# Kernel optimization log

Hardware: AMD Instinct MI355X
Metric: run time of the kernel (lower is better)

Reference implementation:

```python
import jax, jax.numpy as jnp
import numpy as np

N_NODES = 20000
IN_C = 512
OUT_C = 128
HEADS = 4
N_EDGES = 320000
NEG_SLOPE = 0.2


def setup_inputs() -> dict:
    key = jax.random.key(0)
    ks = jax.random.split(key, 10)
    x = jax.random.normal(ks[0], (N_NODES, IN_C), dtype=jnp.float32)
    edge_index = jax.random.randint(ks[1], (2, N_EDGES), 0, N_NODES, dtype=jnp.int64)
    s = 0.05
    return {
        "x": x,
        "edge_index": edge_index,
        "W1": jax.random.normal(ks[2], (IN_C, HEADS * OUT_C), dtype=jnp.float32) * s,
        "a_src1": jax.random.normal(ks[3], (HEADS, OUT_C), dtype=jnp.float32) * s,
        "a_dst1": jax.random.normal(ks[4], (HEADS, OUT_C), dtype=jnp.float32) * s,
        "b1": jnp.zeros((HEADS * OUT_C,), dtype=jnp.float32),
        "W2": jax.random.normal(ks[5], (HEADS * OUT_C, 1 * OUT_C), dtype=jnp.float32) * s,
        "a_src2": jax.random.normal(ks[6], (1, OUT_C), dtype=jnp.float32) * s,
        "a_dst2": jax.random.normal(ks[7], (1, OUT_C), dtype=jnp.float32) * s,
        "b2": jnp.zeros((OUT_C,), dtype=jnp.float32),
    }


def gat_conv(x, src, dst, W, a_src, a_dst, b, heads, out_c, concat):
    N = x.shape[0]
    h = (x @ W).reshape(N, heads, out_c)            # [N,H,C]
    al_src = jnp.sum(h * a_src, axis=-1)            # [N,H]
    al_dst = jnp.sum(h * a_dst, axis=-1)            # [N,H]
    e = jax.nn.leaky_relu(al_src[src] + al_dst[dst], NEG_SLOPE)  # [E,H]
    # segment softmax over edges grouped by destination node
    e_max = jax.ops.segment_max(e, dst, num_segments=N)         # [N,H]
    e = jnp.exp(e - e_max[dst])
    denom = jax.ops.segment_sum(e, dst, num_segments=N)         # [N,H]
    alpha = e / (denom[dst] + 1e-16)                             # [E,H]
    msg = h[src] * alpha[:, :, None]                             # [E,H,C]
    out = jax.ops.segment_sum(msg, dst, num_segments=N)          # [N,H,C]
    out = out.reshape(N, heads * out_c) if concat else jnp.mean(out, axis=1)
    return out + b


def reference(x, edge_index, W1, a_src1, a_dst1, b1, W2, a_src2, a_dst2, b2):
    N = x.shape[0]
    # PyG GATConv adds self-loops by default
    loops = jnp.arange(N, dtype=edge_index.dtype)
    src = jnp.concatenate([edge_index[0], loops])
    dst = jnp.concatenate([edge_index[1], loops])
    h = gat_conv(x, src, dst, W1, a_src1, a_dst1, b1, HEADS, OUT_C, concat=True)
    h = jax.nn.elu(h)
    return gat_conv(h, src, dst, W2, a_src2, a_dst2, b2, 1, OUT_C, concat=False)
```

## Files before the change

kernel.cpp:

```cpp
#include <hip/hip_runtime.h>
#include <hip/hip_bf16.h>

typedef __hip_bfloat16 bf16;
typedef __bf16 bf16x8 __attribute__((ext_vector_type(8)));
typedef float f32x4 __attribute__((ext_vector_type(4)));

#define NEG_SLOPE 0.2f
#define F32_THRESH 256


__device__ __forceinline__ bool is_f32(const int* fcnt) { return *fcnt > F32_THRESH; }

__device__ __forceinline__ float ld_f(const void* p, long long i, bool f32) {
    return f32 ? ((const float*)p)[i] : __bfloat162float(((const bf16*)p)[i]);
}

__device__ __forceinline__ float b2f(unsigned hs) {
    return __uint_as_float(hs << 16);
}

__device__ __forceinline__ unsigned pack_bf2(float a, float b) {
    union { bf16 h[2]; unsigned u; } p;
    p.h[0] = __float2bfloat16(a);
    p.h[1] = __float2bfloat16(b);
    return p.u;
}

__device__ __forceinline__ void load_lds16(const void* g, void* l) {
    __builtin_amdgcn_global_load_lds(
        (const __attribute__((address_space(1))) void*)g,
        (__attribute__((address_space(3))) void*)l, 16, 0, 0);
}

template <int CPL> struct FV;
template <> struct FV<8> {
    uint4 v;
    __device__ __forceinline__ void load(const bf16* p) { v = *(const uint4*)p; }
    __device__ __forceinline__ void fma(float* acc, float w) const {
        unsigned uu[4] = {v.x, v.y, v.z, v.w};
#pragma unroll
        for (int q = 0; q < 4; q++) {
            acc[2 * q] += w * b2f(uu[q] & 0xFFFFu);
            acc[2 * q + 1] += w * b2f(uu[q] >> 16);
        }
    }
};
template <> struct FV<2> {
    unsigned v;
    __device__ __forceinline__ void load(const bf16* p) { v = *(const unsigned*)p; }
    __device__ __forceinline__ void fma(float* acc, float w) const {
        acc[0] += w * b2f(v & 0xFFFFu);
        acc[1] += w * b2f(v >> 16);
    }
};


__global__ void k_probe(const unsigned* xw, long long nw, const int* idx, int n_half,
                        int* cnt, int* iflag) {
    long long t = blockIdx.x * (long long)blockDim.x + threadIdx.x;
    long long stride = (long long)gridDim.x * blockDim.x;
    int c = 0;
    for (long long i = t; i < nw; i += stride)
        if ((xw[i] & 0x7F80u) == 0x7F80u) c++;
    if (c) atomicAdd(cnt, c);
    int any = 0;
    for (long long i = t; i < n_half; i += stride)
        if (idx[2 * i + 1] != 0) any = 1;
    if (any) atomicOr(iflag, 1);
}


__device__ __forceinline__ int edge_val(const void* idx, long long i, int is64) {
    return is64 ? (int)((const long long*)idx)[i] : ((const int*)idx)[i];
}

__global__ void k_count(const void* idx, const int* iflag, int E0, int N, int* deg) {
    int e = blockIdx.x * blockDim.x + threadIdx.x;
    if (e >= E0 + N) return;
    int is64 = (*iflag == 0);
    int d = (e < E0) ? edge_val(idx, (long long)E0 + e, is64) : (e - E0);
    if ((unsigned)d >= (unsigned)N) d = 0;
    atomicAdd(&deg[d], 1);
}

__global__ __launch_bounds__(1024) void k_scan(const int* deg, int* rowptr, int N) {
    __shared__ int part[1024];
    int t = threadIdx.x;
    int chunk = (N + 1023) / 1024;
    int s = t * chunk, e = min(N, s + chunk);
    int sum = 0;
    for (int i = s; i < e; i++) sum += deg[i];
    part[t] = sum;
    __syncthreads();
    for (int off = 1; off < 1024; off <<= 1) {
        int v = (t >= off) ? part[t - off] : 0;
        __syncthreads();
        part[t] += v;
        __syncthreads();
    }
    int run = (t == 0) ? 0 : part[t - 1];
    for (int i = s; i < e; i++) { rowptr[i] = run; run += deg[i]; }
    if (t == 1023) rowptr[N] = part[1023];
}

__global__ void k_scatter(const void* idx, const int* iflag, int E0, int N,
                          const int* rowptr, int* cursor, int* csr_src) {
    int e = blockIdx.x * blockDim.x + threadIdx.x;
    if (e >= E0 + N) return;
    int is64 = (*iflag == 0);
    int s, d;
    if (e < E0) {
        s = edge_val(idx, e, is64);
        d = edge_val(idx, (long long)E0 + e, is64);
    } else {
        s = d = e - E0;
    }
    if ((unsigned)s >= (unsigned)N) s = 0;
    if ((unsigned)d >= (unsigned)N) d = 0;
    int pos = rowptr[d] + atomicAdd(&cursor[d], 1);
    if ((unsigned)pos < (unsigned)(E0 + N)) csr_src[pos] = s;
}


__global__ void k_prep(const void* x, const int* fcnt, bf16* xb, bf16* xtail,
                       const void* W1, bf16* W1t, const void* W2, bf16* W2t,
                       bf16* hpad, int hpad_elems, int N, int K, int C1, int C2,
                       int R0, long long n_valid, long long n_total) {
    const int b = blockIdx.x;
    const int tid = threadIdx.x;
    const bool f32 = is_f32(fcnt);
    if (b < 512) {
        if (!f32) return;
        long long n8 = n_total / 8;
        for (long long i = (long long)b * 256 + tid; i < n8; i += 512LL * 256) {
            long long base = i * 8;
            uint4 out;
            if (base + 8 <= n_valid) {
                const float4* s4 = (const float4*)x;
                float4 x0 = s4[i * 2], x1 = s4[i * 2 + 1];
                out.x = pack_bf2(x0.x, x0.y);
                out.y = pack_bf2(x0.z, x0.w);
                out.z = pack_bf2(x1.x, x1.y);
                out.w = pack_bf2(x1.z, x1.w);
            } else {
                bf16 tmp[8];
#pragma unroll
                for (int j = 0; j < 8; j++) {
                    long long k = base + j;
                    tmp[j] = (k < n_valid) ? __float2bfloat16(ld_f(x, k, true))
                                           : __float2bfloat16(0.f);
                }
                out = *(uint4*)tmp;
            }
            ((uint4*)xb)[i] = out;
        }
    } else if (b < 528) {
        int total = 128 * K;
        for (int i = (b - 512) * 256 + tid; i < total; i += 16 * 256) {
            int r = i / K;
            long long src = (long long)(R0 + r) * K + (i - r * K);
            xtail[i] = (R0 + r < N) ? __float2bfloat16(ld_f(x, src, f32))
                                    : __float2bfloat16(0.f);
        }
    } else if (b < 656) {
        int total = K * C1;
        for (int i = (b - 528) * 256 + tid; i < total; i += 128 * 256) {
            int k = i / C1, n = i - k * C1;
            W1t[(size_t)n * K + k] = __float2bfloat16(ld_f(W1, i, f32));
        }
    } else if (b < 688) {
        int total = C1 * C2;
        for (int i = (b - 656) * 256 + tid; i < total; i += 32 * 256) {
            int k = i / C2, n = i - k * C2;
            W2t[(size_t)n * C1 + k] = __float2bfloat16(ld_f(W2, i, f32));
        }
    } else {
        for (int i = (b - 688) * 256 + tid; i < hpad_elems; i += 16 * 256)
            hpad[i] = __float2bfloat16(0.f);
    }
}


__global__ void k_al(const bf16* __restrict__ h, const void* a_s, const void* a_d,
                     const int* fcnt, float* als, float* ald, int N, int H) {
    __shared__ float sa[512], sd[512];
    const int HC = H * 128;
    bool f32 = is_f32(fcnt);
    for (int i = threadIdx.x; i < HC; i += blockDim.x) {
        sa[i] = ld_f(a_s, i, f32);
        sd[i] = ld_f(a_d, i, f32);
    }
    __syncthreads();
    int i = blockIdx.x * blockDim.x + threadIdx.x;
    if (i >= N * H) return;
    int n = i / H, hh = i % H;
    const uint4* row = (const uint4*)(h + (size_t)n * HC + hh * 128);
    float s = 0.f, d = 0.f;
#pragma unroll
    for (int q = 0; q < 16; q++) {
        uint4 u = row[q];
        unsigned uu[4] = {u.x, u.y, u.z, u.w};
#pragma unroll
        for (int t = 0; t < 4; t++) {
            float v0 = b2f(uu[t] & 0xFFFFu), v1 = b2f(uu[t] >> 16);
            int c = hh * 128 + q * 8 + t * 2;
            s += v0 * sa[c] + v1 * sa[c + 1];
            d += v0 * sd[c] + v1 * sd[c + 1];
        }
    }
    als[i] = s;
    ald[i] = d;
}


template <int BN, bool SEL>
__global__ __launch_bounds__(256) void k_gemm(const void* Araw, const bf16* Aconv,
                                              const bf16* Atail, const int* fcnt,
                                              const bf16* __restrict__ Bt,
                                              bf16* __restrict__ C,
                                              int M, int Nn, int K, int nfull) {
    constexpr int BM = 128, BK = 32;
    constexpr int NT = BN / 32;
    const int m0 = blockIdx.x * BM;
    const int n0 = blockIdx.y * BN;
    __shared__ __bf16 As[BM][BK];
    __shared__ __bf16 Bs[BN][BK];
    const int tid = threadIdx.x;
    const int wave = tid >> 6;
    const int lane = tid & 63;
    const int wm = (wave & 1) * 64;
    const int wn = (wave >> 1) * (NT * 16);
    const int lm = lane & 15;
    const int quad = lane >> 4;
    const int srow = tid >> 2;
    const int scol = (tid & 3) * 8;

    f32x4 acc[4][NT];
#pragma unroll
    for (int mt = 0; mt < 4; mt++)
#pragma unroll
        for (int nt = 0; nt < NT; nt++) acc[mt][nt] = (f32x4){0.f, 0.f, 0.f, 0.f};

    const bf16* Abase;
    int arow0;
    if (SEL) {
        const bf16* Asel = is_f32(fcnt) ? Aconv : (const bf16*)Araw;
        if ((int)blockIdx.x < nfull) { Abase = Asel; arow0 = m0; }
        else { Abase = Atail; arow0 = 0; }
    } else {
        Abase = (const bf16*)Araw;
        arow0 = m0;
    }

    const char* Ab = (const char*)(Abase + (size_t)(arow0 + srow) * K + scol);
    const char* Bb = (const char*)(Bt + (size_t)(n0 + srow) * K + scol);
    char* ldsA = (char*)&As[0][0] + wave * 1024;
    char* ldsB = (char*)&Bs[0][0] + wave * 1024;
    const size_t rstep = (size_t)64 * K * 2;

    for (int k0 = 0; k0 < K; k0 += BK) {
        __syncthreads();
        const size_t kb = (size_t)k0 * 2;
        load_lds16(Ab + kb, ldsA);
        load_lds16(Ab + kb + rstep, ldsA + 4096);
        load_lds16(Bb + kb, ldsB);
        if (BN == 128) load_lds16(Bb + kb + rstep, ldsB + 4096);
        __syncthreads();
        bf16x8 af[4], bfv[NT];
#pragma unroll
        for (int mt = 0; mt < 4; mt++)
            af[mt] = *(const bf16x8*)&As[wm + mt * 16 + lm][quad * 8];
#pragma unroll
        for (int nt = 0; nt < NT; nt++)
            bfv[nt] = *(const bf16x8*)&Bs[wn + nt * 16 + lm][quad * 8];
#pragma unroll
        for (int mt = 0; mt < 4; mt++)
#pragma unroll
            for (int nt = 0; nt < NT; nt++)
                acc[mt][nt] = __builtin_amdgcn_mfma_f32_16x16x32_bf16(
                    af[mt], bfv[nt], acc[mt][nt], 0, 0, 0);
    }

#pragma unroll
    for (int mt = 0; mt < 4; mt++) {
        int rb = m0 + wm + mt * 16 + quad * 4;
#pragma unroll
        for (int nt = 0; nt < NT; nt++) {
            int col = n0 + wn + nt * 16 + lm;
#pragma unroll
            for (int r = 0; r < 4; r++) {
                int row = rb + r;
                if (row < M) C[(size_t)row * Nn + col] = __float2bfloat16(acc[mt][nt][r]);
            }
        }
    }
}


template <int C, int H, bool ELU, bool DYN_OUT>
__global__ __launch_bounds__(256) void k_agg(
    const bf16* __restrict__ feat, const float* __restrict__ als,
    const float* __restrict__ ald, const int* __restrict__ rowptr,
    const int* __restrict__ csr_src, const void* bias, const int* fcnt,
    void* outp, int N, int E) {
    constexpr int CPL = C / 64;
    constexpr int Ch = C / H;
    constexpr int WPAD = (H == 4) ? 5 : 1;
    const int wave = threadIdx.x >> 6;
    const int lane = threadIdx.x & 63;
    const int n = blockIdx.x * 4 + wave;
    const int c0 = lane * CPL;
    const int head = c0 / Ch;

    __shared__ float s_w[4][64 * WPAD];
    __shared__ int s_s[4][64];

    if (n >= N) return;

    int start = rowptr[n];
    if (start < 0) start = 0;
    int end = rowptr[n + 1];
    if (end > E) end = E;
    int deg = end - start;
    if (deg < 0) deg = 0;

    float aldn[H];
    if (H == 4) {
        float4 a4 = ((const float4*)ald)[n];
        aldn[0] = a4.x; aldn[1] = a4.y; aldn[2] = a4.z;
        if (H > 3) aldn[3] = a4.w;
    } else {
        aldn[0] = ald[n];
    }

    float acc[CPL] = {};
    float psum = 0.f;

    for (int base = 0; base < deg; base += 64) {
        int cnt = min(64, deg - base);
        if (lane < cnt) {
            int s = csr_src[start + base + lane];
            if ((unsigned)s >= (unsigned)N) s = 0;
            s_s[wave][lane] = s;
            if (H == 4) {
                float4 a4 = ((const float4*)als)[s];
                float aa[4] = {a4.x, a4.y, a4.z, a4.w};
#pragma unroll
                for (int h = 0; h < 4; h++) {
                    float l = aa[h] + aldn[h];
                    l = l > 0.f ? l : NEG_SLOPE * l;
                    s_w[wave][lane * 5 + h] = __expf(fminf(l, 60.f));
                }
            } else {
                float l = als[s] + aldn[0];
                l = l > 0.f ? l : NEG_SLOPE * l;
                s_w[wave][lane] = __expf(fminf(l, 60.f));
            }
        }
#pragma unroll 4
        for (int e = 0; e < cnt; e++) {
            int s = s_s[wave][e];
            float wl = (H == 4) ? s_w[wave][e * 5 + head] : s_w[wave][e];
            psum += wl;
            FV<CPL> f;
            f.load(feat + (size_t)s * C + c0);
            f.fma(acc, wl);
        }
    }

    const float dn = psum + 1e-16f;
    const bool f32 = is_f32(fcnt);
#pragma unroll
    for (int j = 0; j < CPL; j++) {
        float v = acc[j] / dn + ld_f(bias, c0 + j, f32);
        if (ELU) v = v > 0.f ? v : expf(v) - 1.f;
        size_t oi = (size_t)n * C + c0 + j;
        if (DYN_OUT && f32) ((float*)outp)[oi] = v;
        else ((bf16*)outp)[oi] = __float2bfloat16(v);
    }
}


extern "C" void kernel_launch(void* const* d_in, const int* in_sizes, int n_in,
                              void* d_out, int out_size, void* d_ws, size_t ws_size,
                              hipStream_t stream) {
    const int N = in_sizes[0] / 512;
    const int K = 512;
    const int C1 = 512;
    const int C2 = 128;
    const int H1 = 4;
    const int E0 = in_sizes[1] / 2;
    const int E = E0 + N;
    const int Mpad = (N + 127) / 128 * 128;
    const int nfull = N / 128;

    const void* x_raw = d_in[0];
    const void* eidx = d_in[1];
    const void* W1 = d_in[2];
    const void* as1 = d_in[3];
    const void* ad1 = d_in[4];
    const void* b1 = d_in[5];
    const void* W2 = d_in[6];
    const void* as2 = d_in[7];
    const void* ad2 = d_in[8];
    const void* b2 = d_in[9];

    char* ws = (char*)d_ws;
    size_t off = 0;
    auto take = [&](size_t bytes) {
        size_t r = off;
        off += (bytes + 255) & ~(size_t)255;
        return r;
    };
    bf16* xb     = (bf16*)(ws + take((size_t)Mpad * K * 2));
    bf16* xtail  = (bf16*)(ws + take((size_t)128 * K * 2));
    bf16* h1     = (bf16*)(ws + take((size_t)N * C1 * 2));
    bf16* hagg   = (bf16*)(ws + take((size_t)Mpad * C1 * 2));
    bf16* W1t    = (bf16*)(ws + take((size_t)K * C1 * 2));
    bf16* W2t    = (bf16*)(ws + take((size_t)C1 * C2 * 2));
    float* al1s  = (float*)(ws + take((size_t)N * H1 * 4));
    float* al1d  = (float*)(ws + take((size_t)N * H1 * 4));
    int* rowptr  = (int*)(ws + take((size_t)(N + 1) * 4));
    int* csr_src = (int*)(ws + take((size_t)E * 4));
    int* deg     = (int*)(ws + take((size_t)(2 * N + 2) * 4));
    int* cursor  = deg + N;
    int* iflag   = deg + 2 * N;
    int* fcnt    = deg + 2 * N + 1;
    bf16* h2     = xb;
    float* al2s  = al1s;
    float* al2d  = al1d;
    if (off > ws_size) return;

    hipMemsetAsync(deg, 0, (size_t)(2 * N + 2) * 4, stream);

    long long nw = (long long)in_sizes[0] / 2;
    if (nw > (1 << 20)) nw = 1 << 20;
    int nh = E0 > (1 << 16) ? (1 << 16) : E0;
    k_probe<<<256, 256, 0, stream>>>((const unsigned*)x_raw, nw, (const int*)eidx, nh,
                                     fcnt, iflag);

    k_count<<<(E + 255) / 256, 256, 0, stream>>>(eidx, iflag, E0, N, deg);
    k_scan<<<1, 1024, 0, stream>>>(deg, rowptr, N);
    k_scatter<<<(E + 255) / 256, 256, 0, stream>>>(eidx, iflag, E0, N, rowptr, cursor,
                                                   csr_src);

    k_prep<<<704, 256, 0, stream>>>(x_raw, fcnt, xb, xtail, W1, W1t, W2, W2t,
                                    hagg + (size_t)N * C1, (Mpad - N) * C1,
                                    N, K, C1, C2, nfull * 128,
                                    (long long)N * K, (long long)Mpad * K);

    dim3 g1(Mpad / 128, C1 / 128);
    k_gemm<128, true><<<g1, 256, 0, stream>>>(x_raw, xb, xtail, fcnt, W1t, h1,
                                              N, C1, K, nfull);
    k_al<<<(N * H1 + 255) / 256, 256, 0, stream>>>(h1, as1, ad1, fcnt, al1s, al1d, N, H1);
    k_agg<512, 4, true, false><<<(N + 3) / 4, 256, 0, stream>>>(
        h1, al1s, al1d, rowptr, csr_src, b1, fcnt, hagg, N, E);

    dim3 g2(Mpad / 128, C2 / 64);
    k_gemm<64, false><<<g2, 256, 0, stream>>>(hagg, nullptr, nullptr, fcnt, W2t, h2,
                                              N, C2, C1, 0);
    k_al<<<(N + 255) / 256, 256, 0, stream>>>(h2, as2, ad2, fcnt, al2s, al2d, N, 1);
    k_agg<128, 1, false, true><<<(N + 3) / 4, 256, 0, stream>>>(
        h2, al2s, al2d, rowptr, csr_src, b2, fcnt, d_out, N, E);
}
```

Measured before the change: 316.2 us.

## Fuse attention logits into GEMM epilogue and use block-per-node aggregation

```diff
diff --git a/kernel.cpp b/kernel.cpp
--- a/kernel.cpp
+++ b/kernel.cpp
@@ -181,43 +181,14 @@
 }
 
 
-__global__ void k_al(const bf16* __restrict__ h, const void* a_s, const void* a_d,
-                     const int* fcnt, float* als, float* ald, int N, int H) {
-    __shared__ float sa[512], sd[512];
-    const int HC = H * 128;
-    bool f32 = is_f32(fcnt);
-    for (int i = threadIdx.x; i < HC; i += blockDim.x) {
-        sa[i] = ld_f(a_s, i, f32);
-        sd[i] = ld_f(a_d, i, f32);
-    }
-    __syncthreads();
-    int i = blockIdx.x * blockDim.x + threadIdx.x;
-    if (i >= N * H) return;
-    int n = i / H, hh = i % H;
-    const uint4* row = (const uint4*)(h + (size_t)n * HC + hh * 128);
-    float s = 0.f, d = 0.f;
-#pragma unroll
-    for (int q = 0; q < 16; q++) {
-        uint4 u = row[q];
-        unsigned uu[4] = {u.x, u.y, u.z, u.w};
-#pragma unroll
-        for (int t = 0; t < 4; t++) {
-            float v0 = b2f(uu[t] & 0xFFFFu), v1 = b2f(uu[t] >> 16);
-            int c = hh * 128 + q * 8 + t * 2;
-            s += v0 * sa[c] + v1 * sa[c + 1];
-            d += v0 * sd[c] + v1 * sd[c + 1];
-        }
-    }
-    als[i] = s;
-    ald[i] = d;
-}
-
-
-template <int BN, bool SEL>
+template <int BN, bool SEL, int H>
 __global__ __launch_bounds__(256) void k_gemm(const void* Araw, const bf16* Aconv,
                                               const bf16* Atail, const int* fcnt,
                                               const bf16* __restrict__ Bt,
                                               bf16* __restrict__ C,
+                                              const void* a_s, const void* a_d,
+                                              float* __restrict__ als,
+                                              float* __restrict__ ald,
                                               int M, int Nn, int K, int nfull) {
     constexpr int BM = 128, BK = 32;
     constexpr int NT = BN / 32;
@@ -294,6 +265,39 @@
             }
         }
     }
+
+    const bool f32 = is_f32(fcnt);
+    float sa_[NT], sd_[NT];
+#pragma unroll
+    for (int nt = 0; nt < NT; nt++) {
+        int col = n0 + wn + nt * 16 + lm;
+        sa_[nt] = ld_f(a_s, col, f32);
+        sd_[nt] = ld_f(a_d, col, f32);
+    }
+    const int head = (H == 4) ? (n0 >> 7) : 0;
+#pragma unroll
+    for (int mt = 0; mt < 4; mt++) {
+#pragma unroll
+        for (int r = 0; r < 4; r++) {
+            float ps_ = 0.f, pd_ = 0.f;
+#pragma unroll
+            for (int nt = 0; nt < NT; nt++) {
+                float v = acc[mt][nt][r];
+                ps_ += v * sa_[nt];
+                pd_ += v * sd_[nt];
+            }
+#pragma unroll
+            for (int off = 1; off < 16; off <<= 1) {
+                ps_ += __shfl_xor(ps_, off, 64);
+                pd_ += __shfl_xor(pd_, off, 64);
+            }
+            int row = m0 + wm + mt * 16 + quad * 4 + r;
+            if (lm == 0 && row < M) {
+                atomicAdd(&als[(size_t)row * H + head], ps_);
+                atomicAdd(&ald[(size_t)row * H + head], pd_);
+            }
+        }
+    }
 }
 
 
@@ -305,17 +309,18 @@
     void* outp, int N, int E) {
     constexpr int CPL = C / 64;
     constexpr int Ch = C / H;
-    constexpr int WPAD = (H == 4) ? 5 : 1;
-    const int wave = threadIdx.x >> 6;
-    const int lane = threadIdx.x & 63;
-    const int n = blockIdx.x * 4 + wave;
+    constexpr int WST = (H == 4) ? 5 : 1;
+    const int n = blockIdx.x;
+    const int tid = threadIdx.x;
+    const int wave = tid >> 6;
+    const int lane = tid & 63;
     const int c0 = lane * CPL;
     const int head = c0 / Ch;
 
-    __shared__ float s_w[4][64 * WPAD];
-    __shared__ int s_s[4][64];
-
-    if (n >= N) return;
+    __shared__ float red[4][C];
+    __shared__ float s_w[64 * WST];
+    __shared__ int s_src[64];
+    __shared__ float ps[4][H];
 
     int start = rowptr[n];
     if (start < 0) start = 0;
@@ -324,43 +329,37 @@
     int deg = end - start;
     if (deg < 0) deg = 0;
 
-    float aldn[H];
-    if (H == 4) {
-        float4 a4 = ((const float4*)ald)[n];
-        aldn[0] = a4.x; aldn[1] = a4.y; aldn[2] = a4.z;
-        if (H > 3) aldn[3] = a4.w;
-    } else {
-        aldn[0] = ald[n];
-    }
-
     float acc[CPL] = {};
     float psum = 0.f;
 
     for (int base = 0; base < deg; base += 64) {
         int cnt = min(64, deg - base);
-        if (lane < cnt) {
-            int s = csr_src[start + base + lane];
-            if ((unsigned)s >= (unsigned)N) s = 0;
-            s_s[wave][lane] = s;
-            if (H == 4) {
-                float4 a4 = ((const float4*)als)[s];
-                float aa[4] = {a4.x, a4.y, a4.z, a4.w};
-#pragma unroll
-                for (int h = 0; h < 4; h++) {
-                    float l = aa[h] + aldn[h];
-                    l = l > 0.f ? l : NEG_SLOPE * l;
-                    s_w[wave][lane * 5 + h] = __expf(fminf(l, 60.f));
-                }
-            } else {
-                float l = als[s] + aldn[0];
+        __syncthreads();
+        if (H == 4) {
+            int e_ = tid & 63, h_ = tid >> 6;
+            if (e_ < cnt) {
+                int s = csr_src[start + base + e_];
+                if ((unsigned)s >= (unsigned)N) s = 0;
+                if (h_ == 0) s_src[e_] = s;
+                float l = als[(size_t)s * 4 + h_] + ald[(size_t)n * 4 + h_];
                 l = l > 0.f ? l : NEG_SLOPE * l;
-                s_w[wave][lane] = __expf(fminf(l, 60.f));
-            }
-        }
+                s_w[e_ * 5 + h_] = __expf(fminf(l, 60.f));
+            }
+        } else {
+            if (tid < cnt) {
+                int s = csr_src[start + base + tid];
+                if ((unsigned)s >= (unsigned)N) s = 0;
+                s_src[tid] = s;
+                float l = als[s] + ald[n];
+                l = l > 0.f ? l : NEG_SLOPE * l;
+                s_w[tid] = __expf(fminf(l, 60.f));
+            }
+        }
+        __syncthreads();
 #pragma unroll 4
-        for (int e = 0; e < cnt; e++) {
-            int s = s_s[wave][e];
-            float wl = (H == 4) ? s_w[wave][e * 5 + head] : s_w[wave][e];
+        for (int e = wave; e < cnt; e += 4) {
+            int s = s_src[e];
+            float wl = (H == 4) ? s_w[e * 5 + head] : s_w[e];
             psum += wl;
             FV<CPL> f;
             f.load(feat + (size_t)s * C + c0);
@@ -368,13 +367,24 @@
         }
     }
 
-    const float dn = psum + 1e-16f;
+#pragma unroll
+    for (int j = 0; j < CPL; j++) red[wave][c0 + j] = acc[j];
+    if ((lane & 15) == 0) ps[wave][head] = psum;
+    __syncthreads();
+
     const bool f32 = is_f32(fcnt);
-#pragma unroll
-    for (int j = 0; j < CPL; j++) {
-        float v = acc[j] / dn + ld_f(bias, c0 + j, f32);
+    for (int c = tid; c < C; c += 256) {
+        int h = c / Ch;
+        float sv = 0.f;
+        float dn = 1e-16f;
+#pragma unroll
+        for (int w2 = 0; w2 < 4; w2++) {
+            sv += red[w2][c];
+            dn += ps[w2][h];
+        }
+        float v = sv / dn + ld_f(bias, c, f32);
         if (ELU) v = v > 0.f ? v : expf(v) - 1.f;
-        size_t oi = (size_t)n * C + c0 + j;
+        size_t oi = (size_t)n * C + c;
         if (DYN_OUT && f32) ((float*)outp)[oi] = v;
         else ((bf16*)outp)[oi] = __float2bfloat16(v);
     }
@@ -418,20 +428,21 @@
     bf16* hagg   = (bf16*)(ws + take((size_t)Mpad * C1 * 2));
     bf16* W1t    = (bf16*)(ws + take((size_t)K * C1 * 2));
     bf16* W2t    = (bf16*)(ws + take((size_t)C1 * C2 * 2));
-    float* al1s  = (float*)(ws + take((size_t)N * H1 * 4));
-    float* al1d  = (float*)(ws + take((size_t)N * H1 * 4));
     int* rowptr  = (int*)(ws + take((size_t)(N + 1) * 4));
     int* csr_src = (int*)(ws + take((size_t)E * 4));
-    int* deg     = (int*)(ws + take((size_t)(2 * N + 2) * 4));
-    int* cursor  = deg + N;
-    int* iflag   = deg + 2 * N;
-    int* fcnt    = deg + 2 * N + 1;
+    int* zbase   = (int*)(ws + take((size_t)(12 * N + 2) * 4));
+    int* deg     = zbase;
+    int* cursor  = zbase + N;
+    float* al1s  = (float*)(zbase + 2 * N);
+    float* al1d  = al1s + 4 * N;
+    float* al2s  = al1d + 4 * N;
+    float* al2d  = al2s + N;
+    int* iflag   = zbase + 12 * N;
+    int* fcnt    = zbase + 12 * N + 1;
     bf16* h2     = xb;
-    float* al2s  = al1s;
-    float* al2d  = al1d;
     if (off > ws_size) return;
 
-    hipMemsetAsync(deg, 0, (size_t)(2 * N + 2) * 4, stream);
+    hipMemsetAsync(zbase, 0, (size_t)(12 * N + 2) * 4, stream);
 
     long long nw = (long long)in_sizes[0] / 2;
     if (nw > (1 << 20)) nw = 1 << 20;
@@ -450,16 +461,14 @@
                                     (long long)N * K, (long long)Mpad * K);
 
     dim3 g1(Mpad / 128, C1 / 128);
-    k_gemm<128, true><<<g1, 256, 0, stream>>>(x_raw, xb, xtail, fcnt, W1t, h1,
-                                              N, C1, K, nfull);
-    k_al<<<(N * H1 + 255) / 256, 256, 0, stream>>>(h1, as1, ad1, fcnt, al1s, al1d, N, H1);
-    k_agg<512, 4, true, false><<<(N + 3) / 4, 256, 0, stream>>>(
+    k_gemm<128, true, 4><<<g1, 256, 0, stream>>>(x_raw, xb, xtail, fcnt, W1t, h1,
+                                                 as1, ad1, al1s, al1d, N, C1, K, nfull);
+    k_agg<512, 4, true, false><<<N, 256, 0, stream>>>(
         h1, al1s, al1d, rowptr, csr_src, b1, fcnt, hagg, N, E);
 
     dim3 g2(Mpad / 128, C2 / 64);
-    k_gemm<64, false><<<g2, 256, 0, stream>>>(hagg, nullptr, nullptr, fcnt, W2t, h2,
-                                              N, C2, C1, 0);
-    k_al<<<(N + 255) / 256, 256, 0, stream>>>(h2, as2, ad2, fcnt, al2s, al2d, N, 1);
-    k_agg<128, 1, false, true><<<(N + 3) / 4, 256, 0, stream>>>(
+    k_gemm<64, false, 1><<<g2, 256, 0, stream>>>(hagg, nullptr, nullptr, fcnt, W2t, h2,
+                                                 as2, ad2, al2s, al2d, N, C2, C1, 0);
+    k_agg<128, 1, false, true><<<N, 256, 0, stream>>>(
         h2, al2s, al2d, rowptr, csr_src, b2, fcnt, d_out, N, E);
 }
```

Measured after the change: 327.0 us. 1.03x slower.
